# Kernel tuning notes

Hardware: AMD Instinct MI355X
Metric: run time of the kernel (lower is better)

The kernel has to match this reference:

```python
import jax, jax.numpy as jnp
import numpy as np

N = 100000
E = 1600000
CUR = 128
HID = 128
OUT = 128

def setup_inputs() -> dict:
    key = jax.random.key(0)
    ks = jax.random.split(key, 12)
    s = 1.0 / np.sqrt(HID)
    return {
        "x": jax.random.normal(ks[0], (N, CUR), dtype=jnp.float32),
        "edge_index": jax.random.randint(ks[1], (2, E), 0, N, dtype=jnp.int64),
        "edge_weight": jax.random.uniform(ks[2], (E,), dtype=jnp.float32),
        # preprocessor Linear(cur_dim -> hidden_dim), stored as [in, out]
        "W_pre": jax.random.normal(ks[3], (CUR, HID), dtype=jnp.float32) * s,
        "b_pre": jnp.zeros((HID,), dtype=jnp.float32),
        # ARMAConv(hidden -> out), num_stacks=1, num_layers=1 defaults
        "arma_init_w": jax.random.normal(ks[4], (HID, OUT), dtype=jnp.float32) * s,
        "arma_root_w": jax.random.normal(ks[5], (HID, OUT), dtype=jnp.float32) * s,
        "arma_b": jnp.zeros((OUT,), dtype=jnp.float32),
        # SAGEConv(hidden -> out): lin_l on aggregated neighbors (with bias), lin_r on root
        "sage_l_w": jax.random.normal(ks[6], (HID, OUT), dtype=jnp.float32) * s,
        "sage_l_b": jnp.zeros((OUT,), dtype=jnp.float32),
        "sage_r_w": jax.random.normal(ks[7], (HID, OUT), dtype=jnp.float32) * s,
    }

def reference(x, edge_index, edge_weight, W_pre, b_pre, arma_init_w, arma_root_w,
              arma_b, sage_l_w, sage_l_b, sage_r_w):
    row, col = edge_index[0], edge_index[1]  # source -> target

    # preprocessor
    h = x @ W_pre + b_pre  # [N, HID]

    # ---- ARMAConv (num_stacks=1, num_layers=1, act=ReLU) ----
    # gcn_norm without self-loops
    deg = jax.ops.segment_sum(edge_weight, col, num_segments=N)  # in-degree (weighted)
    dis = jnp.where(deg > 0, jax.lax.rsqrt(jnp.maximum(deg, 1e-12)), 0.0)
    norm = dis[row] * edge_weight * dis[col]  # [E]
    t = h @ arma_init_w  # [N, OUT]
    agg = jax.ops.segment_sum(norm[:, None] * t[row], col, num_segments=N)
    arma_out = jax.nn.relu(agg + h @ arma_root_w + arma_b)

    # ---- SAGEConv (mean aggregation, weighted messages, root term) ----
    msg_sum = jax.ops.segment_sum(edge_weight[:, None] * h[row], col, num_segments=N)
    cnt = jax.ops.segment_sum(jnp.ones((E,), dtype=h.dtype), col, num_segments=N)
    mean = msg_sum / jnp.maximum(cnt, 1.0)[:, None]
    sage_out = mean @ sage_l_w + sage_l_b + h @ sage_r_w

    h1 = jax.nn.leaky_relu(arma_out, negative_slope=0.01)
    h2 = jax.nn.leaky_relu(sage_out, negative_slope=0.01)
    return jax.nn.elu(jnp.concatenate([h1, h2], axis=1))
```

## Files before the change

### kernel.cpp

```cpp
#include <hip/hip_runtime.h>
#include <math.h>


typedef __attribute__((ext_vector_type(8))) short short8;
typedef __attribute__((ext_vector_type(4))) float float4v;

#define WQ_SCALE 32767.0f
#define WQ_INV   (1.0f / 32767.0f)
#define NB_BIN   256

__device__ __forceinline__ unsigned f2bf_pack(float a, float b) {
    unsigned ua = __float_as_uint(a);
    unsigned ub = __float_as_uint(b);
    ua += 0x7FFF + ((ua >> 16) & 1);
    ub += 0x7FFF + ((ub >> 16) & 1);
    return (ua >> 16) | (ub & 0xFFFF0000u);
}

__device__ __forceinline__ unsigned short f2bf1(float a) {
    unsigned u = __float_as_uint(a);
    u += 0x7FFF + ((u >> 16) & 1);
    return (unsigned short)(u >> 16);
}

__device__ __forceinline__ float act_leaky_elu(float v) {
    float l = (v >= 0.0f) ? v : 0.01f * v;
    return (l > 0.0f) ? l : expm1f(l);
}

__device__ __forceinline__ short8 load_bfrag(const float* __restrict__ W,
                                             int n, int k0) {
    union { short8 s8; unsigned u[4]; } r;
    #pragma unroll
    for (int j = 0; j < 4; ++j) {
        float a = W[(k0 + 2 * j) * 128 + n];
        float b = W[(k0 + 2 * j + 1) * 128 + n];
        r.u[j] = f2bf_pack(a, b);
    }
    return r.s8;
}

__device__ __forceinline__ short8 load_afrag_f32(const float* __restrict__ p) {
    float4 a = ((const float4*)p)[0];
    float4 b = ((const float4*)p)[1];
    union { short8 s8; unsigned u[4]; } r;
    r.u[0] = f2bf_pack(a.x, a.y); r.u[1] = f2bf_pack(a.z, a.w);
    r.u[2] = f2bf_pack(b.x, b.y); r.u[3] = f2bf_pack(b.z, b.w);
    return r.s8;
}

__device__ __forceinline__ void gemm_pre(const float* __restrict__ x,
                                         const float* __restrict__ Wpre,
                                         const float* __restrict__ bpre,
                                         unsigned short* __restrict__ hb,
                                         int N) {
    const int lane = threadIdx.x & 63;
    const int wv = threadIdx.x >> 6;
    const int q = lane >> 4;
    const int m = lane & 15;
    const int cg = wv * 32;
    short8 B[2][4];
    #pragma unroll
    for (int ct = 0; ct < 2; ++ct)
        #pragma unroll
        for (int c = 0; c < 4; ++c)
            B[ct][c] = load_bfrag(Wpre, cg + ct * 16 + m, c * 32 + q * 8);
    const float b0 = bpre[cg + m];
    const float b1 = bpre[cg + 16 + m];
    const int rb = blockIdx.x * 128;
    #pragma unroll 2
    for (int rt = 0; rt < 8; ++rt) {
        int row = rb + rt * 16 + m;
        int rc = min(row, N - 1);
        const float* xp = x + (size_t)rc * 128 + q * 8;
        float4v a0 = {0.f, 0.f, 0.f, 0.f}, a1 = {0.f, 0.f, 0.f, 0.f};
        #pragma unroll
        for (int c = 0; c < 4; ++c) {
            short8 a = load_afrag_f32(xp + c * 32);
            a0 = __builtin_amdgcn_mfma_f32_16x16x32_bf16(a, B[0][c], a0, 0, 0, 0);
            a1 = __builtin_amdgcn_mfma_f32_16x16x32_bf16(a, B[1][c], a1, 0, 0, 0);
        }
        #pragma unroll
        for (int r = 0; r < 4; ++r) {
            int ro = rb + rt * 16 + q * 4 + r;
            if (ro < N) {
                hb[(size_t)ro * 128 + cg + m]      = f2bf1(a0[r] + b0);
                hb[(size_t)ro * 128 + cg + 16 + m] = f2bf1(a1[r] + b1);
            }
        }
    }
}

__global__ __launch_bounds__(256)
void k_pre_bin1(const float* __restrict__ x, const float* __restrict__ Wpre,
                const float* __restrict__ bpre, unsigned short* __restrict__ hb,
                int N, int gd,
                const int* __restrict__ ei, int* __restrict__ gcnt,
                unsigned* __restrict__ aux, int* __restrict__ bbase,
                int E, int NBKT) {
    __shared__ int hist[1024];
    if ((int)blockIdx.x >= gd) {
        const int cb = (int)blockIdx.x - gd;
        const int tid = threadIdx.x;
        for (int j = tid; j < NBKT; j += 256) hist[j] = 0;
        __syncthreads();
        const int stride = NB_BIN * 256;
        for (int e = cb * 256 + tid; e < E; e += stride) {
            int col = ei[E + e];
            aux[e] = (unsigned)atomicAdd(&hist[col >> 7], 1);
        }
        __syncthreads();
        for (int j = tid; j < NBKT; j += 256) {
            int h = hist[j];
            int bb = (h > 0) ? atomicAdd(&gcnt[j], h) : 0;
            bbase[cb * 1024 + j] = bb;
        }
        return;
    }
    gemm_pre(x, Wpre, bpre, hb, N);
}

__global__ __launch_bounds__(256)
void k_pre_cntD(const float* __restrict__ x, const float* __restrict__ Wpre,
                const float* __restrict__ bpre, unsigned short* __restrict__ hb,
                int N, int gd,
                const int* __restrict__ ei, int* __restrict__ cnti,
                int* __restrict__ rank, int E) {
    if ((int)blockIdx.x >= gd) {
        const int stride = ((int)gridDim.x - gd) * 256;
        for (int e = ((int)blockIdx.x - gd) * 256 + (int)threadIdx.x; e < E;
             e += stride) {
            rank[e] = atomicAdd(&cnti[ei[E + e]], 1);
        }
        return;
    }
    gemm_pre(x, Wpre, bpre, hb, N);
}

__global__ __launch_bounds__(256)
void k_scan1(const int* __restrict__ in, int* __restrict__ out,
             int* __restrict__ blksum, int n) {
    __shared__ int sh[256];
    const int tid = threadIdx.x;
    const int idx = blockIdx.x * 1024 + tid * 4;
    int v0 = (idx + 0 < n) ? in[idx + 0] : 0;
    int v1 = (idx + 1 < n) ? in[idx + 1] : 0;
    int v2 = (idx + 2 < n) ? in[idx + 2] : 0;
    int v3 = (idx + 3 < n) ? in[idx + 3] : 0;
    int tsum = v0 + v1 + v2 + v3;
    sh[tid] = tsum;
    __syncthreads();
    #pragma unroll
    for (int off = 1; off < 256; off <<= 1) {
        int add = (tid >= off) ? sh[tid - off] : 0;
        __syncthreads();
        sh[tid] += add;
        __syncthreads();
    }
    int excl = sh[tid] - tsum;
    if (idx + 0 < n) out[idx + 0] = excl;
    if (idx + 1 < n) out[idx + 1] = excl + v0;
    if (idx + 2 < n) out[idx + 2] = excl + v0 + v1;
    if (idx + 3 < n) out[idx + 3] = excl + v0 + v1 + v2;
    if (tid == 255) blksum[blockIdx.x] = sh[255];
}

__global__ __launch_bounds__(128)
void k_scan2(int* __restrict__ blksum, int nb) {
    __shared__ int sh[128];
    const int tid = threadIdx.x;
    int orig = (tid < nb) ? blksum[tid] : 0;
    sh[tid] = orig;
    __syncthreads();
    #pragma unroll
    for (int off = 1; off < 128; off <<= 1) {
        int add = (tid >= off) ? sh[tid - off] : 0;
        __syncthreads();
        sh[tid] += add;
        __syncthreads();
    }
    if (tid < nb) blksum[tid] = sh[tid] - orig;
}

__global__ __launch_bounds__(256)
void k_bin2(const int* __restrict__ ei, const float* __restrict__ ew,
            const unsigned* __restrict__ aux, const int* __restrict__ gbase,
            const int* __restrict__ bbase, uint2* __restrict__ binned,
            int E, int NBKT) {
    __shared__ int base[1024];
    const int cb = blockIdx.x;
    const int tid = threadIdx.x;
    for (int j = tid; j < NBKT; j += 256)
        base[j] = gbase[j] + bbase[cb * 1024 + j];
    __syncthreads();
    const int stride = NB_BIN * 256;
    for (int e = cb * 256 + tid; e < E; e += stride) {
        int col = ei[E + e];
        int src = ei[e];
        unsigned wq = (unsigned)__builtin_rintf(ew[e] * WQ_SCALE) & 0x7FFFu;
        int pos = base[col >> 7] + (int)aux[e];
        binned[pos] = make_uint2((wq << 17) | (unsigned)src, (unsigned)col);
    }
}

__global__ __launch_bounds__(256)
void k_bktcsr(const uint2* __restrict__ binned, const int* __restrict__ gbase,
              unsigned* __restrict__ recs, int* __restrict__ rowp,
              float* __restrict__ dis, int N, int E) {
    __shared__ int cnt[128];
    __shared__ int colbase[128];
    __shared__ unsigned long long wsum[128];
    const int bkt = blockIdx.x;
    const int tid = threadIdx.x;
    if (tid < 128) { cnt[tid] = 0; wsum[tid] = 0ULL; }
    __syncthreads();
    const int s = gbase[bkt], e = gbase[bkt + 1];
    for (int i = s + tid; i < e; i += 256) {
        uint2 r = binned[i];
        int cl = (int)(r.y & 127u);
        atomicAdd(&cnt[cl], 1);
        atomicAdd(&wsum[cl], (unsigned long long)(r.x >> 17));
    }
    __syncthreads();
    if (tid < 128) colbase[tid] = cnt[tid];
    __syncthreads();
    #pragma unroll
    for (int off = 1; off < 128; off <<= 1) {
        int add = 0;
        if (tid < 128 && tid >= off) add = colbase[tid - off];
        __syncthreads();
        if (tid < 128) colbase[tid] += add;
        __syncthreads();
    }
    if (tid < 128) {
        colbase[tid] = s + colbase[tid] - cnt[tid];
        int node = bkt * 128 + tid;
        if (node < N) {
            rowp[node] = colbase[tid];
            float d = (float)wsum[tid] * WQ_INV;
            dis[node] = (wsum[tid] > 0ULL)
                          ? (1.0f / sqrtf(fmaxf(d, 1e-12f))) : 0.0f;
        }
        cnt[tid] = 0;
    }
    if (bkt == 0 && tid == 0) rowp[N] = E;
    __syncthreads();
    for (int i = s + tid; i < e; i += 256) {
        uint2 r = binned[i];
        int cl = (int)(r.y & 127u);
        int rk = atomicAdd(&cnt[cl], 1);
        recs[colbase[cl] + rk] = r.x;
    }
}

__global__ __launch_bounds__(256)
void k_scatterW(const int* __restrict__ ei, const float* __restrict__ ew,
                const int* __restrict__ rowp, const int* __restrict__ blks,
                const int* __restrict__ rank, int2* __restrict__ recs, int E) {
    int e = blockIdx.x * 256 + threadIdx.x;
    if (e < E) {
        int c = ei[E + e];
        int pos = rowp[c] + blks[c >> 10] + rank[e];
        recs[pos] = make_int2(ei[e], __float_as_int(ew[e]));
    }
}

__global__ __launch_bounds__(256)
void k_degsumW(const int* __restrict__ rowp, const int* __restrict__ blks,
               const int2* __restrict__ recs, float* __restrict__ dis, int N) {
    int n = blockIdx.x * 256 + threadIdx.x;
    if (n >= N) return;
    int s  = rowp[n] + blks[n >> 10];
    int eE = rowp[n + 1] + blks[(n + 1) >> 10];
    float d = 0.0f;
    for (int e = s; e < eE; ++e) d += __int_as_float(recs[e].y);
    dis[n] = (d > 0.0f) ? (1.0f / sqrtf(fmaxf(d, 1e-12f))) : 0.0f;
}

template <bool ABS>
__global__ __launch_bounds__(256)
void k_pull(const int* __restrict__ rowp, const int* __restrict__ blks,
            const void* __restrict__ recs_, const float* __restrict__ dis,
            const uint4* __restrict__ hb4, uint4* __restrict__ agb4,
            uint4* __restrict__ mnb4, int N) {
    const int node = blockIdx.x * 4 + (threadIdx.x >> 6);
    if (node >= N) return;
    const int lane = threadIdx.x & 63;
    const int q4 = lane >> 4;
    const int sub = lane & 15;
    int s, eE;
    if (ABS) {
        s  = __builtin_amdgcn_readfirstlane(rowp[node]);
        eE = __builtin_amdgcn_readfirstlane(rowp[node + 1]);
    } else {
        s  = __builtin_amdgcn_readfirstlane(rowp[node] + blks[node >> 10]);
        eE = __builtin_amdgcn_readfirstlane(rowp[node + 1] +
                                            blks[(node + 1) >> 10]);
    }
    const float dcol = dis[node];
    const float im = 1.0f / fmaxf((float)(eE - s), 1.0f);

    float aA[8], aM[8];
    #pragma unroll
    for (int i = 0; i < 8; ++i) { aA[i] = 0.f; aM[i] = 0.f; }

    #pragma unroll 2
    for (int e = s; e < eE; e += 4) {
        int el = e + q4;
        bool ok = el < eE;
        int el2 = ok ? el : (eE - 1);
        int src; float w;
        if (ABS) {
            unsigned rv = ((const unsigned*)recs_)[el2];
            src = (int)(rv & 0x1FFFFu);
            w = (float)(rv >> 17) * WQ_INV;
        } else {
            int2 rv = ((const int2*)recs_)[el2];
            src = rv.x;
            w = __int_as_float(rv.y);
        }
        if (!ok) w = 0.f;
        float c = dis[src] * w;
        uint4 u = hb4[(size_t)src * 16 + sub];
        float f0 = __uint_as_float(u.x << 16);
        float f1 = __uint_as_float(u.x & 0xFFFF0000u);
        float f2 = __uint_as_float(u.y << 16);
        float f3 = __uint_as_float(u.y & 0xFFFF0000u);
        float f4 = __uint_as_float(u.z << 16);
        float f5 = __uint_as_float(u.z & 0xFFFF0000u);
        float f6 = __uint_as_float(u.w << 16);
        float f7 = __uint_as_float(u.w & 0xFFFF0000u);
        aA[0] = fmaf(c, f0, aA[0]); aM[0] = fmaf(w, f0, aM[0]);
        aA[1] = fmaf(c, f1, aA[1]); aM[1] = fmaf(w, f1, aM[1]);
        aA[2] = fmaf(c, f2, aA[2]); aM[2] = fmaf(w, f2, aM[2]);
        aA[3] = fmaf(c, f3, aA[3]); aM[3] = fmaf(w, f3, aM[3]);
        aA[4] = fmaf(c, f4, aA[4]); aM[4] = fmaf(w, f4, aM[4]);
        aA[5] = fmaf(c, f5, aA[5]); aM[5] = fmaf(w, f5, aM[5]);
        aA[6] = fmaf(c, f6, aA[6]); aM[6] = fmaf(w, f6, aM[6]);
        aA[7] = fmaf(c, f7, aA[7]); aM[7] = fmaf(w, f7, aM[7]);
    }

    #pragma unroll
    for (int i = 0; i < 8; ++i) {
        aA[i] += __shfl_xor(aA[i], 32, 64);
        aA[i] += __shfl_xor(aA[i], 16, 64);
        aM[i] += __shfl_xor(aM[i], 32, 64);
        aM[i] += __shfl_xor(aM[i], 16, 64);
    }

    if (q4 == 0) {
        uint4 o;
        o.x = f2bf_pack(aA[0] * dcol, aA[1] * dcol);
        o.y = f2bf_pack(aA[2] * dcol, aA[3] * dcol);
        o.z = f2bf_pack(aA[4] * dcol, aA[5] * dcol);
        o.w = f2bf_pack(aA[6] * dcol, aA[7] * dcol);
        agb4[(size_t)node * 16 + sub] = o;
    } else if (q4 == 1) {
        uint4 o;
        o.x = f2bf_pack(aM[0] * im, aM[1] * im);
        o.y = f2bf_pack(aM[2] * im, aM[3] * im);
        o.z = f2bf_pack(aM[4] * im, aM[5] * im);
        o.w = f2bf_pack(aM[6] * im, aM[7] * im);
        mnb4[(size_t)node * 16 + sub] = o;
    }
}

__global__ __launch_bounds__(512)
void k_final2(const unsigned short* __restrict__ agb,
              const unsigned short* __restrict__ mnb,
              const unsigned short* __restrict__ hb,
              const float* __restrict__ Wai, const float* __restrict__ War,
              const float* __restrict__ ab,
              const float* __restrict__ Wsl, const float* __restrict__ Wsr,
              const float* __restrict__ bsl,
              float* __restrict__ out, int N) {
    const int lane = threadIdx.x & 63;
    const int wv = threadIdx.x >> 6;
    const bool sg = wv >= 4;
    const int q = lane >> 4;
    const int m = lane & 15;
    const int cg = (wv & 3) * 32;
    const unsigned short* A1 = sg ? mnb : agb;
    const float* W1 = sg ? Wsl : Wai;
    const float* W2 = sg ? Wsr : War;
    const float* bias = sg ? bsl : ab;
    float* op = out + (sg ? 128 : 0);
    short8 B1[2][4], B2[2][4];
    #pragma unroll
    for (int ct = 0; ct < 2; ++ct)
        #pragma unroll
        for (int c = 0; c < 4; ++c) {
            B1[ct][c] = load_bfrag(W1, cg + ct * 16 + m, c * 32 + q * 8);
            B2[ct][c] = load_bfrag(W2, cg + ct * 16 + m, c * 32 + q * 8);
        }
    const float b0 = bias[cg + m];
    const float b1 = bias[cg + 16 + m];
    const int rb = blockIdx.x * 128;
    #pragma unroll 2
    for (int rt = 0; rt < 8; ++rt) {
        int row = rb + rt * 16 + m;
        int rc = min(row, N - 1);
        const short8* a1 = (const short8*)(A1 + (size_t)rc * 128 + q * 8);
        const short8* a2 = (const short8*)(hb + (size_t)rc * 128 + q * 8);
        float4v c0 = {0.f, 0.f, 0.f, 0.f}, c1 = {0.f, 0.f, 0.f, 0.f};
        #pragma unroll
        for (int c = 0; c < 4; ++c) {
            short8 a = a1[c * 4];
            c0 = __builtin_amdgcn_mfma_f32_16x16x32_bf16(a, B1[0][c], c0, 0, 0, 0);
            c1 = __builtin_amdgcn_mfma_f32_16x16x32_bf16(a, B1[1][c], c1, 0, 0, 0);
        }
        #pragma unroll
        for (int c = 0; c < 4; ++c) {
            short8 a = a2[c * 4];
            c0 = __builtin_amdgcn_mfma_f32_16x16x32_bf16(a, B2[0][c], c0, 0, 0, 0);
            c1 = __builtin_amdgcn_mfma_f32_16x16x32_bf16(a, B2[1][c], c1, 0, 0, 0);
        }
        #pragma unroll
        for (int r = 0; r < 4; ++r) {
            int ro = rb + rt * 16 + q * 4 + r;
            if (ro < N) {
                float v0 = c0[r] + b0;
                float v1 = c1[r] + b1;
                if (!sg) { v0 = fmaxf(v0, 0.f); v1 = fmaxf(v1, 0.f); }
                else     { v0 = act_leaky_elu(v0); v1 = act_leaky_elu(v1); }
                op[(size_t)ro * 256 + cg + m]      = v0;
                op[(size_t)ro * 256 + cg + 16 + m] = v1;
            }
        }
    }
}

extern "C" void kernel_launch(void* const* d_in, const int* in_sizes, int n_in,
                              void* d_out, int out_size, void* d_ws, size_t ws_size,
                              hipStream_t stream) {
    const float* x    = (const float*)d_in[0];
    const int*   ei   = (const int*)d_in[1];
    const float* ew   = (const float*)d_in[2];
    const float* Wpre = (const float*)d_in[3];
    const float* bpre = (const float*)d_in[4];
    const float* Wai  = (const float*)d_in[5];
    const float* War  = (const float*)d_in[6];
    const float* ab   = (const float*)d_in[7];
    const float* Wsl  = (const float*)d_in[8];
    const float* bsl  = (const float*)d_in[9];
    const float* Wsr  = (const float*)d_in[10];

    const int N = in_sizes[0] / 128;
    const int E = in_sizes[2];
    const size_t NF = (size_t)N * 128;
    const int NBKT = (N + 127) >> 7;
    const bool packed = (N <= 130944);

    char* p = (char*)d_ws;
    auto take = [&p](size_t bytes) {
        char* r = p;
        p += (bytes + 255) & ~(size_t)255;
        return r;
    };
    unsigned short* hb  = (unsigned short*)take(NF * 2);
    unsigned short* agb = (unsigned short*)take(NF * 2);
    unsigned short* mnb = (unsigned short*)take(NF * 2);
    unsigned* recs = (unsigned*)take(packed ? (size_t)E * 4 : (size_t)E * 8);
    int*   rowp = (int*)take((size_t)(N + 1) * 4);
    float* dis  = (float*)take((size_t)N * 4);
    int*   cti  = (int*)take((size_t)(N + 1) * 4);
    int*   blks = (int*)take(128 * 4);
    int*   gcnt  = (int*)take(1025 * 4);
    int*   gbase = (int*)take(1025 * 4);

    size_t binB = (size_t)E * 8;
    uint2* binned = (NF * 2 >= binB) ? (uint2*)agb : (uint2*)take(binB);
    size_t auxB = ((size_t)E * 4 + 255) & ~(size_t)255;
    size_t bbB  = (size_t)NB_BIN * 1024 * 4;
    unsigned* aux; int* bbase;
    if (NF * 2 >= auxB + bbB) {
        aux = (unsigned*)mnb;
        bbase = (int*)((char*)mnb + auxB);
    } else {
        aux = (unsigned*)take((size_t)E * 4);
        bbase = (int*)take(bbB);
    }

    const int gd = (N + 127) / 128;
    const int ge = (E + 255) / 256;
    const int gv = (N + 255) / 256;
    const int ns = N + 1;
    const int nb = (ns + 1023) / 1024;

    if (packed) {
        hipMemsetAsync(gcnt, 0, (size_t)(NBKT + 1) * 4, stream);
        k_pre_bin1<<<gd + NB_BIN, 256, 0, stream>>>(x, Wpre, bpre, hb, N, gd,
                                                    ei, gcnt, aux, bbase,
                                                    E, NBKT);
        k_scan1<<<1, 256, 0, stream>>>(gcnt, gbase, blks, NBKT + 1);
        k_bin2<<<NB_BIN, 256, 0, stream>>>(ei, ew, aux, gbase, bbase,
                                           binned, E, NBKT);
        k_bktcsr<<<NBKT, 256, 0, stream>>>(binned, gbase, recs, rowp, dis,
                                           N, E);
        k_pull<true><<<(N + 3) / 4, 256, 0, stream>>>(rowp, blks, recs, dis,
            (const uint4*)hb, (uint4*)agb, (uint4*)mnb, N);
    } else {
        hipMemsetAsync(cti, 0, (size_t)(N + 1) * 4, stream);
        k_pre_cntD<<<gd + 2048, 256, 0, stream>>>(x, Wpre, bpre, hb, N, gd,
                                                  ei, cti, (int*)aux, E);
        k_scan1<<<nb, 256, 0, stream>>>(cti, rowp, blks, ns);
        k_scan2<<<1, 128, 0, stream>>>(blks, nb);
        k_scatterW<<<ge, 256, 0, stream>>>(ei, ew, rowp, blks, (int*)aux,
                                           (int2*)recs, E);
        k_degsumW<<<gv, 256, 0, stream>>>(rowp, blks, (const int2*)recs,
                                          dis, N);
        k_pull<false><<<(N + 3) / 4, 256, 0, stream>>>(rowp, blks, recs, dis,
            (const uint4*)hb, (uint4*)agb, (uint4*)mnb, N);
    }

    k_final2<<<gd, 512, 0, stream>>>(agb, mnb, hb, Wai, War, ab,
                                     Wsl, Wsr, bsl, (float*)d_out, N);
}
```

Measured before the change: 383.3 us.

## Prepack bf16 weight fragments, fold bucket scan into consumers, retile final GEMM

Adds a small prep kernel that converts all five weight matrices into bf16 MFMA B-fragment layout once, so the GEMM kernels load one uint4 per fragment instead of eight strided fp32 loads plus conversion. The separate single-block scan launch is removed: k_bin2 and k_bktcsr each recompute the 1024-entry exclusive scan of bucket counts in shared memory. The final GEMM halves rows per block to double the grid and splits accumulators to interleave the two products. It also swaps expm1f for __expf-1, which is less accurate near zero. Redundant per-block scans add work, and the prep kernel adds a launch.

```diff
diff --git a/kernel.cpp b/kernel.cpp
--- a/kernel.cpp
+++ b/kernel.cpp
@@ -25,19 +25,14 @@
 
 __device__ __forceinline__ float act_leaky_elu(float v) {
     float l = (v >= 0.0f) ? v : 0.01f * v;
-    return (l > 0.0f) ? l : expm1f(l);
-}
-
-__device__ __forceinline__ short8 load_bfrag(const float* __restrict__ W,
-                                             int n, int k0) {
-    union { short8 s8; unsigned u[4]; } r;
-    #pragma unroll
-    for (int j = 0; j < 4; ++j) {
-        float a = W[(k0 + 2 * j) * 128 + n];
-        float b = W[(k0 + 2 * j + 1) * 128 + n];
-        r.u[j] = f2bf_pack(a, b);
-    }
-    return r.s8;
+    return (l > 0.0f) ? l : (__expf(l) - 1.0f);
+}
+
+__device__ __forceinline__ short8 ldfrag(const uint4* __restrict__ pw,
+                                         int n, int c, int q) {
+    union { uint4 u; short8 s; } r;
+    r.u = pw[(size_t)(c * 128 + n) * 4 + q];
+    return r.s;
 }
 
 __device__ __forceinline__ short8 load_afrag_f32(const float* __restrict__ p) {
@@ -49,8 +44,27 @@
     return r.s8;
 }
 
+__global__ __launch_bounds__(256)
+void k_prep(const float* __restrict__ W0, const float* __restrict__ W1,
+            const float* __restrict__ W2, const float* __restrict__ W3,
+            const float* __restrict__ W4, uint4* __restrict__ pw) {
+    const int mat = blockIdx.x;
+    const float* W = (mat == 0) ? W0 : (mat == 1) ? W1 : (mat == 2) ? W2
+                   : (mat == 3) ? W3 : W4;
+    for (int f = threadIdx.x; f < 2048; f += 256) {
+        int q = f & 3, n = (f >> 2) & 127, c = f >> 9;
+        int k0 = c * 32 + q * 8;
+        unsigned u[4];
+        #pragma unroll
+        for (int j = 0; j < 4; ++j)
+            u[j] = f2bf_pack(W[(k0 + 2 * j) * 128 + n],
+                             W[(k0 + 2 * j + 1) * 128 + n]);
+        pw[(size_t)mat * 2048 + f] = make_uint4(u[0], u[1], u[2], u[3]);
+    }
+}
+
 __device__ __forceinline__ void gemm_pre(const float* __restrict__ x,
-                                         const float* __restrict__ Wpre,
+                                         const uint4* __restrict__ pw,
                                          const float* __restrict__ bpre,
                                          unsigned short* __restrict__ hb,
                                          int N) {
@@ -64,7 +78,7 @@
     for (int ct = 0; ct < 2; ++ct)
         #pragma unroll
         for (int c = 0; c < 4; ++c)
-            B[ct][c] = load_bfrag(Wpre, cg + ct * 16 + m, c * 32 + q * 8);
+            B[ct][c] = ldfrag(pw, cg + ct * 16 + m, c, q);
     const float b0 = bpre[cg + m];
     const float b1 = bpre[cg + 16 + m];
     const int rb = blockIdx.x * 128;
@@ -92,7 +106,7 @@
 }
 
 __global__ __launch_bounds__(256)
-void k_pre_bin1(const float* __restrict__ x, const float* __restrict__ Wpre,
+void k_pre_bin1(const float* __restrict__ x, const uint4* __restrict__ pw,
                 const float* __restrict__ bpre, unsigned short* __restrict__ hb,
                 int N, int gd,
                 const int* __restrict__ ei, int* __restrict__ gcnt,
@@ -117,11 +131,11 @@
         }
         return;
     }
-    gemm_pre(x, Wpre, bpre, hb, N);
-}
-
-__global__ __launch_bounds__(256)
-void k_pre_cntD(const float* __restrict__ x, const float* __restrict__ Wpre,
+    gemm_pre(x, pw, bpre, hb, N);
+}
+
+__global__ __launch_bounds__(256)
+void k_pre_cntD(const float* __restrict__ x, const uint4* __restrict__ pw,
                 const float* __restrict__ bpre, unsigned short* __restrict__ hb,
                 int N, int gd,
                 const int* __restrict__ ei, int* __restrict__ cnti,
@@ -134,7 +148,29 @@
         }
         return;
     }
-    gemm_pre(x, Wpre, bpre, hb, N);
+    gemm_pre(x, pw, bpre, hb, N);
+}
+
+__device__ __forceinline__ void scan1024_excl(int* v, int* t) {
+    const int tid = threadIdx.x;
+    int a0 = v[tid * 4 + 0], a1 = v[tid * 4 + 1];
+    int a2 = v[tid * 4 + 2], a3 = v[tid * 4 + 3];
+    int ts = a0 + a1 + a2 + a3;
+    t[tid] = ts;
+    __syncthreads();
+    #pragma unroll
+    for (int off = 1; off < 256; off <<= 1) {
+        int add = (tid >= off) ? t[tid - off] : 0;
+        __syncthreads();
+        t[tid] += add;
+        __syncthreads();
+    }
+    int ex = t[tid] - ts;
+    v[tid * 4 + 0] = ex;
+    v[tid * 4 + 1] = ex + a0;
+    v[tid * 4 + 2] = ex + a0 + a1;
+    v[tid * 4 + 3] = ex + a0 + a1 + a2;
+    __syncthreads();
 }
 
 __global__ __launch_bounds__(256)
@@ -184,14 +220,21 @@
 
 __global__ __launch_bounds__(256)
 void k_bin2(const int* __restrict__ ei, const float* __restrict__ ew,
-            const unsigned* __restrict__ aux, const int* __restrict__ gbase,
+            const unsigned* __restrict__ aux, const int* __restrict__ gcnt,
             const int* __restrict__ bbase, uint2* __restrict__ binned,
             int E, int NBKT) {
     __shared__ int base[1024];
+    __shared__ int tmp[256];
     const int cb = blockIdx.x;
     const int tid = threadIdx.x;
-    for (int j = tid; j < NBKT; j += 256)
-        base[j] = gbase[j] + bbase[cb * 1024 + j];
+    #pragma unroll
+    for (int k = 0; k < 4; ++k) {
+        int i = tid * 4 + k;
+        base[i] = (i < NBKT) ? gcnt[i] : 0;
+    }
+    __syncthreads();
+    scan1024_excl(base, tmp);
+    for (int j = tid; j < NBKT; j += 256) base[j] += bbase[cb * 1024 + j];
     __syncthreads();
     const int stride = NB_BIN * 256;
     for (int e = cb * 256 + tid; e < E; e += stride) {
@@ -204,17 +247,25 @@
 }
 
 __global__ __launch_bounds__(256)
-void k_bktcsr(const uint2* __restrict__ binned, const int* __restrict__ gbase,
+void k_bktcsr(const uint2* __restrict__ binned, const int* __restrict__ gcnt,
               unsigned* __restrict__ recs, int* __restrict__ rowp,
-              float* __restrict__ dis, int N, int E) {
+              float* __restrict__ dis, int N, int E, int NBKT) {
+    __shared__ int gb[1024];
+    __shared__ int tmp[256];
     __shared__ int cnt[128];
     __shared__ int colbase[128];
     __shared__ unsigned long long wsum[128];
     const int bkt = blockIdx.x;
     const int tid = threadIdx.x;
+    #pragma unroll
+    for (int k = 0; k < 4; ++k) {
+        int i = tid * 4 + k;
+        gb[i] = (i < NBKT) ? gcnt[i] : 0;
+    }
     if (tid < 128) { cnt[tid] = 0; wsum[tid] = 0ULL; }
     __syncthreads();
-    const int s = gbase[bkt], e = gbase[bkt + 1];
+    scan1024_excl(gb, tmp);
+    const int s = gb[bkt], e = gb[bkt + 1];
     for (int i = s + tid; i < e; i += 256) {
         uint2 r = binned[i];
         int cl = (int)(r.y & 127u);
@@ -369,10 +420,8 @@
 void k_final2(const unsigned short* __restrict__ agb,
               const unsigned short* __restrict__ mnb,
               const unsigned short* __restrict__ hb,
-              const float* __restrict__ Wai, const float* __restrict__ War,
-              const float* __restrict__ ab,
-              const float* __restrict__ Wsl, const float* __restrict__ Wsr,
-              const float* __restrict__ bsl,
+              const uint4* __restrict__ pw,
+              const float* __restrict__ ab, const float* __restrict__ bsl,
               float* __restrict__ out, int N) {
     const int lane = threadIdx.x & 63;
     const int wv = threadIdx.x >> 6;
@@ -381,8 +430,8 @@
     const int m = lane & 15;
     const int cg = (wv & 3) * 32;
     const unsigned short* A1 = sg ? mnb : agb;
-    const float* W1 = sg ? Wsl : Wai;
-    const float* W2 = sg ? Wsr : War;
+    const uint4* W1 = pw + (size_t)(sg ? 3 : 1) * 2048;
+    const uint4* W2 = pw + (size_t)(sg ? 4 : 2) * 2048;
     const float* bias = sg ? bsl : ab;
     float* op = out + (sg ? 128 : 0);
     short8 B1[2][4], B2[2][4];
@@ -390,37 +439,35 @@
     for (int ct = 0; ct < 2; ++ct)
         #pragma unroll
         for (int c = 0; c < 4; ++c) {
-            B1[ct][c] = load_bfrag(W1, cg + ct * 16 + m, c * 32 + q * 8);
-            B2[ct][c] = load_bfrag(W2, cg + ct * 16 + m, c * 32 + q * 8);
+            B1[ct][c] = ldfrag(W1, cg + ct * 16 + m, c, q);
+            B2[ct][c] = ldfrag(W2, cg + ct * 16 + m, c, q);
         }
     const float b0 = bias[cg + m];
     const float b1 = bias[cg + 16 + m];
-    const int rb = blockIdx.x * 128;
+    const int rb = blockIdx.x * 64;
     #pragma unroll 2
-    for (int rt = 0; rt < 8; ++rt) {
+    for (int rt = 0; rt < 4; ++rt) {
         int row = rb + rt * 16 + m;
         int rc = min(row, N - 1);
         const short8* a1 = (const short8*)(A1 + (size_t)rc * 128 + q * 8);
         const short8* a2 = (const short8*)(hb + (size_t)rc * 128 + q * 8);
-        float4v c0 = {0.f, 0.f, 0.f, 0.f}, c1 = {0.f, 0.f, 0.f, 0.f};
+        float4v c0a = {0.f,0.f,0.f,0.f}, c0b = {0.f,0.f,0.f,0.f};
+        float4v c1a = {0.f,0.f,0.f,0.f}, c1b = {0.f,0.f,0.f,0.f};
         #pragma unroll
         for (int c = 0; c < 4; ++c) {
             short8 a = a1[c * 4];
-            c0 = __builtin_amdgcn_mfma_f32_16x16x32_bf16(a, B1[0][c], c0, 0, 0, 0);
-            c1 = __builtin_amdgcn_mfma_f32_16x16x32_bf16(a, B1[1][c], c1, 0, 0, 0);
-        }
-        #pragma unroll
-        for (int c = 0; c < 4; ++c) {
-            short8 a = a2[c * 4];
-            c0 = __builtin_amdgcn_mfma_f32_16x16x32_bf16(a, B2[0][c], c0, 0, 0, 0);
-            c1 = __builtin_amdgcn_mfma_f32_16x16x32_bf16(a, B2[1][c], c1, 0, 0, 0);
+            short8 b = a2[c * 4];
+            c0a = __builtin_amdgcn_mfma_f32_16x16x32_bf16(a, B1[0][c], c0a, 0, 0, 0);
+            c1a = __builtin_amdgcn_mfma_f32_16x16x32_bf16(a, B1[1][c], c1a, 0, 0, 0);
+            c0b = __builtin_amdgcn_mfma_f32_16x16x32_bf16(b, B2[0][c], c0b, 0, 0, 0);
+            c1b = __builtin_amdgcn_mfma_f32_16x16x32_bf16(b, B2[1][c], c1b, 0, 0, 0);
         }
         #pragma unroll
         for (int r = 0; r < 4; ++r) {
             int ro = rb + rt * 16 + q * 4 + r;
             if (ro < N) {
-                float v0 = c0[r] + b0;
-                float v1 = c1[r] + b1;
+                float v0 = c0a[r] + c0b[r] + b0;
+                float v1 = c1a[r] + c1b[r] + b1;
                 if (!sg) { v0 = fmaxf(v0, 0.f); v1 = fmaxf(v1, 0.f); }
                 else     { v0 = act_leaky_elu(v0); v1 = act_leaky_elu(v1); }
                 op[(size_t)ro * 256 + cg + m]      = v0;
@@ -465,8 +512,8 @@
     float* dis  = (float*)take((size_t)N * 4);
     int*   cti  = (int*)take((size_t)(N + 1) * 4);
     int*   blks = (int*)take(128 * 4);
-    int*   gcnt  = (int*)take(1025 * 4);
-    int*   gbase = (int*)take(1025 * 4);
+    int*   gcnt = (int*)take(1025 * 4);
+    uint4* pw   = (uint4*)take((size_t)5 * 2048 * 16);
 
     size_t binB = (size_t)E * 8;
     uint2* binned = (NF * 2 >= binB) ? (uint2*)agb : (uint2*)take(binB);
@@ -482,26 +529,28 @@
     }
 
     const int gd = (N + 127) / 128;
+    const int gf = (N + 63) / 64;
     const int ge = (E + 255) / 256;
     const int gv = (N + 255) / 256;
     const int ns = N + 1;
     const int nb = (ns + 1023) / 1024;
 
+    k_prep<<<5, 256, 0, stream>>>(Wpre, Wai, War, Wsl, Wsr, pw);
+
     if (packed) {
         hipMemsetAsync(gcnt, 0, (size_t)(NBKT + 1) * 4, stream);
-        k_pre_bin1<<<gd + NB_BIN, 256, 0, stream>>>(x, Wpre, bpre, hb, N, gd,
+        k_pre_bin1<<<gd + NB_BIN, 256, 0, stream>>>(x, pw, bpre, hb, N, gd,
                                                     ei, gcnt, aux, bbase,
                                                     E, NBKT);
-        k_scan1<<<1, 256, 0, stream>>>(gcnt, gbase, blks, NBKT + 1);
-        k_bin2<<<NB_BIN, 256, 0, stream>>>(ei, ew, aux, gbase, bbase,
+        k_bin2<<<NB_BIN, 256, 0, stream>>>(ei, ew, aux, gcnt, bbase,
                                            binned, E, NBKT);
-        k_bktcsr<<<NBKT, 256, 0, stream>>>(binned, gbase, recs, rowp, dis,
-                                           N, E);
+        k_bktcsr<<<NBKT, 256, 0, stream>>>(binned, gcnt, recs, rowp, dis,
+                                           N, E, NBKT);
         k_pull<true><<<(N + 3) / 4, 256, 0, stream>>>(rowp, blks, recs, dis,
             (const uint4*)hb, (uint4*)agb, (uint4*)mnb, N);
     } else {
         hipMemsetAsync(cti, 0, (size_t)(N + 1) * 4, stream);
-        k_pre_cntD<<<gd + 2048, 256, 0, stream>>>(x, Wpre, bpre, hb, N, gd,
+        k_pre_cntD<<<gd + 2048, 256, 0, stream>>>(x, pw, bpre, hb, N, gd,
                                                   ei, cti, (int*)aux, E);
         k_scan1<<<nb, 256, 0, stream>>>(cti, rowp, blks, ns);
         k_scan2<<<1, 128, 0, stream>>>(blks, nb);
@@ -513,6 +562,6 @@
             (const uint4*)hb, (uint4*)agb, (uint4*)mnb, N);
     }
 
-    k_final2<<<gd, 512, 0, stream>>>(agb, mnb, hb, Wai, War, ab,
-                                     Wsl, Wsr, bsl, (float*)d_out, N);
-}
+    k_final2<<<gf, 512, 0, stream>>>(agb, mnb, hb, pw, ab, bsl,
+                                     (float*)d_out, N);
+}
```

After: 373.3 us. 1.03x faster.
